# Kernel tuning notes

Hardware: AMD Instinct MI355X
Metric: run time of the kernel (lower is better)

The kernel has to match this reference:

```python
import jax, jax.numpy as jnp
import numpy as np

B, S, H = 2, 256, 512
EPS = 1e-12  # TPLinker conditional LayerNorm default epsilon
NEG = -1e30  # finite stand-in for -inf in running max


def _cond_layer_norm(x, cond, Wg, Wb, gamma, beta):
    # TPLinker conditional LayerNorm: gamma/beta are modulated by a linear map of cond.
    g = gamma + cond @ Wg          # (..., H)
    b = beta + cond @ Wb           # (..., H)
    xc = x - jnp.mean(x, axis=-1, keepdims=True)
    inv = jax.lax.rsqrt(jnp.mean(xc * xc, axis=-1, keepdims=True) + EPS)
    return xc * inv * g + b


def setup_inputs() -> dict:
    key = jax.random.key(0)
    ks = jax.random.split(key, 6)
    return {
        "seq_hiddens": jax.random.normal(ks[0], (B, S, H), jnp.float32),
        "mask": jnp.ones((B, S), jnp.float32),
        "lamtha": jax.random.uniform(ks[1], (H,), jnp.float32),
        "Wg1": jax.random.normal(ks[2], (H, H), jnp.float32) * 0.02,
        "Wb1": jax.random.normal(ks[3], (H, H), jnp.float32) * 0.02,
        "g1": jnp.ones((H,), jnp.float32),
        "b1": jnp.zeros((H,), jnp.float32),
        "Wg2": jax.random.normal(ks[4], (H, H), jnp.float32) * 0.02,
        "Wb2": jax.random.normal(ks[5], (H, H), jnp.float32) * 0.02,
        "g2": jnp.ones((H,), jnp.float32),
        "b2": jnp.zeros((H,), jnp.float32),
    }


def reference(seq_hiddens, mask, lamtha, Wg1, Wb1, g1, b1, Wg2, Wb2, g2, b2):
    # mask additive penalty, broadcast over hidden (matches (1-mask)*-1000 expand)
    seq = seq_hiddens + ((1.0 - mask) * -1000.0)[:, :, None]  # (B,S,H)

    ii, jj = jnp.triu_indices(S)  # row-major pairs (i, j>=i), same order as the torch loop

    # window means over seq[i..j] via cumulative sums (replaces O(S^3) recomputation)
    csum = jnp.cumsum(seq, axis=1)                              # (B,S,H)
    lens = (jj - ii + 1).astype(seq.dtype)[None, :, None]
    mean_pairs = (csum[:, jj] - csum[:, ii] + seq[:, ii]) / lens  # (B,P,H)

    # window maxes over seq[i..j]: scan over j keeping running max per start i
    idx = jnp.arange(S)

    def step(state, j):
        sj = jnp.take(seq, j, axis=1)  # (B,H)
        new = jnp.where((idx <= j)[None, :, None],
                        jnp.maximum(state, sj[:, None, :]),
                        jnp.asarray(NEG, seq.dtype))
        return new, new

    _, Mall = jax.lax.scan(step, jnp.full((B, S, H), NEG, seq.dtype), idx)  # (S_j,B,S_i,H)
    max_pairs = Mall[jj, :, ii].transpose(1, 0, 2)  # (B,P,H)

    # mix pooling
    inner = lamtha * mean_pairs + (1.0 - lamtha) * max_pairs  # (B,P,H)

    visible = seq[:, jj]  # (B,P,H) token j
    repeat = seq[:, ii]   # (B,P,H) token i

    shaking = _cond_layer_norm(visible, repeat, Wg1, Wb1, g1, b1)
    return _cond_layer_norm(shaking, inner, Wg2, Wb2, g2, b2)
```

## Files before the change

### kernel.cpp

```cpp
#include <hip/hip_runtime.h>
#include <hip/hip_bf16.h>

typedef __hip_bfloat16 bf16;
typedef short short8 __attribute__((ext_vector_type(8)));
typedef float floatx4 __attribute__((ext_vector_type(4)));

#define S 256
#define H 512
#define P 32896
#define NROWS 65792
#define NEGF -1e30f
#define EPSF 1e-12f

#define OFF_LN1    2129920u
#define OFF_G1     3178496u
#define OFF_B1     4227072u
#define OFF_WCAT   5275648u
#define OFF_II     6324224u
#define OFF_JJ     6390016u
#define OFF_MU2    6455808u
#define OFF_INV2   6718976u
#define OFF_INNER  6982144u

__device__ __forceinline__ void gld_lds16(const void* g, void* l) {
    __builtin_amdgcn_global_load_lds(
        (const __attribute__((address_space(1))) void*)g,
        (__attribute__((address_space(3))) void*)l, 16, 0, 0);
}

__global__ __launch_bounds__(512) void fusedA_kernel(
    const float* __restrict__ x, const float* __restrict__ mask,
    float* __restrict__ ln1,
    const float* __restrict__ Wg2, const float* __restrict__ Wb2,
    bf16* __restrict__ wcatT,
    unsigned short* __restrict__ ii, unsigned short* __restrict__ jj) {
    __shared__ float part[8][8][2];
    __shared__ float rstat[8][2];
    if (blockIdx.x < 64) {
        int b = blockIdx.x >> 5, sc = blockIdx.x & 31, h = threadIdx.x;
        int wave = h >> 6, lane = h & 63;
        int s0 = sc * 8;
        float v[8];
#pragma unroll
        for (int t = 0; t < 8; ++t) {
            int s = s0 + t;
            v[t] = x[(size_t)(b * S + s) * H + h] + (1.0f - mask[b * S + s]) * (-1000.0f);
        }
#pragma unroll
        for (int t = 0; t < 8; ++t) {
            float s = v[t], q = v[t] * v[t];
            for (int o = 1; o < 64; o <<= 1) { s += __shfl_xor(s, o); q += __shfl_xor(q, o); }
            if (lane == 0) { part[wave][t][0] = s; part[wave][t][1] = q; }
        }
        __syncthreads();
        if (h < 16) {
            int row = h >> 1, st = h & 1;
            float a = 0.0f;
#pragma unroll
            for (int w = 0; w < 8; ++w) a += part[w][row][st];
            rstat[row][st] = a;
        }
        __syncthreads();
#pragma unroll
        for (int t = 0; t < 8; ++t) {
            float m = rstat[t][0] * (1.0f / 512.0f);
            float var = rstat[t][1] * (1.0f / 512.0f) - m * m;
            var = var < 0.0f ? 0.0f : var;
            float inv = rsqrtf(var + EPSF);
            ln1[(size_t)(b * S + s0 + t) * H + h] = (v[t] - m) * inv;
        }
    } else {
        int n = blockIdx.x - 64;
        if (n < 1024) {
            int k = threadIdx.x;
            int tt = n >> 7, u = n & 127;
            int wnn = u >> 6, v = u & 63;
            int h = tt * 64 + wnn * 32 + (v & 31);
            float val = (v < 32) ? Wg2[(size_t)k * H + h] : Wb2[(size_t)k * H + h];
            wcatT[(size_t)n * H + k] = __float2bfloat16(val);
        } else {
            int p = (n - 1024) * 512 + threadIdx.x;
            if (p >= P) return;
            float disc = 513.0f * 513.0f - 8.0f * (float)p;
            int i = (int)((513.0f - sqrtf(disc)) * 0.5f);
            i = i < 0 ? 0 : (i > S - 1 ? S - 1 : i);
            while (i > 0 && (i * S - i * (i - 1) / 2) > p) --i;
            while (i < S - 1 && ((i + 1) * S - (i + 1) * i / 2) <= p) ++i;
            int off = i * S - i * (i - 1) / 2;
            ii[p] = (unsigned short)i;
            jj[p] = (unsigned short)(i + (p - off));
        }
    }
}

__global__ __launch_bounds__(256) void g1b1_kernel(
    const float* __restrict__ x, const float* __restrict__ mask,
    const float* __restrict__ Wg1, const float* __restrict__ Wb1,
    const float* __restrict__ g1, const float* __restrict__ b1,
    float* __restrict__ G1, float* __restrict__ B1) {
    __shared__ float rowbuf[4][H];
    int grp = blockIdx.x;
    int mat = blockIdx.y;
    int tid = threadIdx.x;
    int h0 = tid, h1 = tid + 256;
    int r0 = grp * 4;
#pragma unroll
    for (int r = 0; r < 4; ++r) {
        int row = r0 + r;
        float add = (1.0f - mask[row]) * (-1000.0f);
        rowbuf[r][h0] = x[(size_t)row * H + h0] + add;
        rowbuf[r][h1] = x[(size_t)row * H + h1] + add;
    }
    __syncthreads();
    const float* W = mat ? Wb1 : Wg1;
    float acc[4][2] = {{0, 0}, {0, 0}, {0, 0}, {0, 0}};
    for (int k8 = 0; k8 < 64; ++k8) {
        float4 ra[4][2];
#pragma unroll
        for (int r = 0; r < 4; ++r) {
            ra[r][0] = ((const float4*)rowbuf[r])[k8 * 2];
            ra[r][1] = ((const float4*)rowbuf[r])[k8 * 2 + 1];
        }
        float w0[8], w1[8];
#pragma unroll
        for (int kk = 0; kk < 8; ++kk) {
            w0[kk] = W[(size_t)(k8 * 8 + kk) * H + h0];
            w1[kk] = W[(size_t)(k8 * 8 + kk) * H + h1];
        }
#pragma unroll
        for (int r = 0; r < 4; ++r) {
            acc[r][0] += ra[r][0].x * w0[0] + ra[r][0].y * w0[1] +
                         ra[r][0].z * w0[2] + ra[r][0].w * w0[3] +
                         ra[r][1].x * w0[4] + ra[r][1].y * w0[5] +
                         ra[r][1].z * w0[6] + ra[r][1].w * w0[7];
            acc[r][1] += ra[r][0].x * w1[0] + ra[r][0].y * w1[1] +
                         ra[r][0].z * w1[2] + ra[r][0].w * w1[3] +
                         ra[r][1].x * w1[4] + ra[r][1].y * w1[5] +
                         ra[r][1].z * w1[6] + ra[r][1].w * w1[7];
        }
    }
    float bias0 = (mat ? b1 : g1)[h0];
    float bias1 = (mat ? b1 : g1)[h1];
    float* dst = mat ? B1 : G1;
#pragma unroll
    for (int r = 0; r < 4; ++r) {
        dst[(size_t)(r0 + r) * H + h0] = acc[r][0] + bias0;
        dst[(size_t)(r0 + r) * H + h1] = acc[r][1] + bias1;
    }
}

__global__ __launch_bounds__(256) void innerstats_kernel(
    const float* __restrict__ x, const float* __restrict__ mask,
    const float* __restrict__ lamtha,
    const float* __restrict__ ln1, const float* __restrict__ G1,
    const float* __restrict__ B1,
    bf16* __restrict__ inner, float* __restrict__ mu2, float* __restrict__ inv2) {
    __shared__ float sh_a[256];
    __shared__ float sh_b[256];
    int id = blockIdx.x;
    int kind = id & 1, sub = id >> 1;
    int t = sub & 255, b = sub >> 8;
    int i = b ? (255 - t) : t;
    int tid = threadIdx.x;
    int off = i * S - i * (i - 1) / 2;

    if (kind == 0) {
        int h2 = tid;
        sh_a[tid] = (1.0f - mask[b * S + tid]) * (-1000.0f);
        sh_b[tid] = 1.0f / (float)(tid + 1);
        __syncthreads();
        float2 lam = ((const float2*)lamtha)[h2];
        float2 oml = {1.0f - lam.x, 1.0f - lam.y};
        const float2* xb = (const float2*)(x + (size_t)b * S * H);
        float2 mrun = {NEGF, NEGF};
        float2 srun = {0.0f, 0.0f};
        size_t base = (size_t)b * P + (size_t)off;
        __hip_bfloat162* dst = (__hip_bfloat162*)inner;
        int j = i;
#define INNER_STEP(xx, jx)                                                 \
    {                                                                      \
        float ma = sh_a[jx];                                               \
        float vx = xx.x + ma, vy = xx.y + ma;                              \
        srun.x += vx;                                                      \
        srun.y += vy;                                                      \
        mrun.x = fmaxf(mrun.x, vx);                                        \
        mrun.y = fmaxf(mrun.y, vy);                                        \
        float rl = sh_b[(jx) - i];                                         \
        float fx = lam.x * (srun.x * rl) + oml.x * mrun.x;                 \
        float fy = lam.y * (srun.y * rl) + oml.y * mrun.y;                 \
        dst[(base + (size_t)((jx) - i)) * 256 + h2] =                      \
            __float22bfloat162_rn(make_float2(fx, fy));                    \
    }
        for (; j + 4 <= S; j += 4) {
            float2 x0 = xb[(j + 0) * 256 + h2];
            float2 x1 = xb[(j + 1) * 256 + h2];
            float2 x2 = xb[(j + 2) * 256 + h2];
            float2 x3 = xb[(j + 3) * 256 + h2];
            INNER_STEP(x0, j + 0)
            INNER_STEP(x1, j + 1)
            INNER_STEP(x2, j + 2)
            INNER_STEP(x3, j + 3)
        }
        for (; j < S; ++j) {
            float2 xv = xb[j * 256 + h2];
            INNER_STEP(xv, j)
        }
#undef INNER_STEP
    } else {
        int wave = tid >> 6, lane = tid & 63;
        const float4* gp = (const float4*)(G1 + (size_t)(b * S + i) * H);
        const float4* bp = (const float4*)(B1 + (size_t)(b * S + i) * H);
        float4 ga = gp[lane * 2], gb = gp[lane * 2 + 1];
        float4 ba = bp[lane * 2], bb = bp[lane * 2 + 1];
        for (int j = i + wave; j < S; j += 4) {
            const float4* lp = (const float4*)(ln1 + (size_t)(b * S + j) * H);
            float4 a0 = lp[lane * 2], a1 = lp[lane * 2 + 1];
            float v0 = a0.x * ga.x + ba.x, v1 = a0.y * ga.y + ba.y;
            float v2 = a0.z * ga.z + ba.z, v3 = a0.w * ga.w + ba.w;
            float v4 = a1.x * gb.x + bb.x, v5 = a1.y * gb.y + bb.y;
            float v6 = a1.z * gb.z + bb.z, v7 = a1.w * gb.w + bb.w;
            float sum = ((v0 + v1) + (v2 + v3)) + ((v4 + v5) + (v6 + v7));
            float ss = ((v0 * v0 + v1 * v1) + (v2 * v2 + v3 * v3)) +
                       ((v4 * v4 + v5 * v5) + (v6 * v6 + v7 * v7));
            for (int o = 1; o < 64; o <<= 1) { sum += __shfl_xor(sum, o); ss += __shfl_xor(ss, o); }
            if (lane == 0) {
                int r = b * P + off + (j - i);
                float m = sum * (1.0f / 512.0f);
                float var = ss * (1.0f / 512.0f) - m * m;
                var = var < 0.0f ? 0.0f : var;
                mu2[r] = m;
                inv2[r] = rsqrtf(var + EPSF);
            }
        }
    }
}

__global__ __launch_bounds__(256, 2) void gemm_kernel(
    const bf16* __restrict__ inner, const bf16* __restrict__ wcatT,
    const float* __restrict__ g2, const float* __restrict__ b2,
    const float* __restrict__ ln1, const float* __restrict__ G1, const float* __restrict__ B1,
    const unsigned short* __restrict__ ii, const unsigned short* __restrict__ jj,
    const float* __restrict__ mu2, const float* __restrict__ inv2,
    float* __restrict__ out) {
    extern __shared__ __align__(16) char smem[];

    const int tid = threadIdx.x;
    const int wave = tid >> 6, lane = tid & 63;
    const int q = lane >> 4, l15 = lane & 15;
    const int wm = wave & 1, wn = wave >> 1;

    const int id = blockIdx.x;
    int rb, t;
    if (id < 2048) { rb = (id >> 6) * 8 + (id & 7); t = (id >> 3) & 7; }
    else           { rb = 256; t = id - 2048; }
    const int R0 = rb * 256;

    int arow[4], acq[4];
#pragma unroll
    for (int s2 = 0; s2 < 4; ++s2) {
        int ci = s2 * 256 + tid;
        int pr = ci >> 3, pc = ci & 7, l = pc ^ (pr & 7);
        arow[s2] = (pr << 1) | (l >> 2);
        acq[s2] = l & 3;
    }
    const bf16* Asrc0 = inner + (size_t)(R0 + arow[0]) * H + acq[0] * 8;
    const bf16* Asrc1 = inner + (size_t)(R0 + arow[1]) * H + acq[1] * 8;
    const bf16* Asrc2 = inner + (size_t)(R0 + arow[2]) * H + acq[2] * 8;
    const bf16* Asrc3 = inner + (size_t)(R0 + arow[3]) * H + acq[3] * 8;
    const bf16* Bsrc0 = wcatT + (size_t)(t * 128 + arow[0]) * H + acq[0] * 8;
    const bf16* Bsrc1 = wcatT + (size_t)(t * 128 + arow[1]) * H + acq[1] * 8;

    char* const A0 = smem;
    char* const B0 = smem + 16384;
    char* const A1 = smem + 24576;
    char* const B1s = smem + 40960;

    const int prl = l15 >> 1;
    const int apc = ((((l15 & 1) << 2) | q) ^ prl) << 4;
    const int C = prl * 128 + apc;

    floatx4 acc[8][4];
#pragma unroll
    for (int a = 0; a < 8; ++a)
#pragma unroll
        for (int c = 0; c < 4; ++c) acc[a][c] = (floatx4){0.f, 0.f, 0.f, 0.f};

    auto STAGE = [&](int kt, char* Ad, char* Bd) {
        gld_lds16(Asrc0 + kt * 32, Ad + 0 * 4096 + wave * 1024);
        gld_lds16(Asrc1 + kt * 32, Ad + 1 * 4096 + wave * 1024);
        gld_lds16(Asrc2 + kt * 32, Ad + 2 * 4096 + wave * 1024);
        gld_lds16(Asrc3 + kt * 32, Ad + 3 * 4096 + wave * 1024);
        gld_lds16(Bsrc0 + kt * 32, Bd + 0 * 4096 + wave * 1024);
        gld_lds16(Bsrc1 + kt * 32, Bd + 1 * 4096 + wave * 1024);
    };

    STAGE(0, A0, B0);
    STAGE(1, A1, B1s);
    asm volatile("s_waitcnt vmcnt(6)" ::: "memory");
    asm volatile("s_barrier" ::: "memory");

#pragma unroll
    for (int kt = 0; kt < 16; ++kt) {
        char* const As = (kt & 1) ? A1 : A0;
        char* const Bs = (kt & 1) ? B1s : B0;

        short8 af[8], bfr[4];
#pragma unroll
        for (int fn = 0; fn < 4; ++fn)
            bfr[fn] = *(const short8*)(Bs + wn * 4096 + fn * 1024 + C);
#pragma unroll
        for (int fm = 0; fm < 8; ++fm)
            af[fm] = *(const short8*)(As + wm * 8192 + fm * 1024 + C);

        __builtin_amdgcn_s_setprio(1);
#pragma unroll
        for (int fm = 0; fm < 4; ++fm)
#pragma unroll
            for (int fn = 0; fn < 4; ++fn)
                acc[fm][fn] = __builtin_amdgcn_mfma_f32_16x16x32_bf16(af[fm], bfr[fn], acc[fm][fn], 0, 0, 0);
        __builtin_amdgcn_s_setprio(0);

        if (kt < 14) {
            asm volatile("s_waitcnt lgkmcnt(0)" ::: "memory");
            asm volatile("s_barrier" ::: "memory");
            STAGE(kt + 2, As, Bs);
        }

        __builtin_amdgcn_s_setprio(1);
#pragma unroll
        for (int fm = 4; fm < 8; ++fm)
#pragma unroll
            for (int fn = 0; fn < 4; ++fn)
                acc[fm][fn] = __builtin_amdgcn_mfma_f32_16x16x32_bf16(af[fm], bfr[fn], acc[fm][fn], 0, 0, 0);
        __builtin_amdgcn_s_setprio(0);

        if (kt < 14) {
            asm volatile("s_waitcnt vmcnt(6)" ::: "memory");
            asm volatile("s_barrier" ::: "memory");
        } else if (kt == 14) {
            asm volatile("s_waitcnt vmcnt(0)" ::: "memory");
            asm volatile("s_barrier" ::: "memory");
        }
    }

    float g2v[2], b2v[2];
#pragma unroll
    for (int fg = 0; fg < 2; ++fg) {
        int h = t * 64 + wn * 32 + fg * 16 + l15;
        g2v[fg] = g2[h];
        b2v[fg] = b2[h];
    }
#pragma unroll
    for (int fm = 0; fm < 8; ++fm) {
#pragma unroll
        for (int r = 0; r < 4; ++r) {
            int m = wm * 128 + fm * 16 + q * 4 + r;
            int rg = R0 + m;
            int b = (rg >= P) ? 1 : 0;
            int p = rg - b * P;
            int i = ii[p], j = jj[p];
            float mu = mu2[rg], iv = inv2[rg];
            const float* lp = ln1 + (size_t)(b * S + j) * H + t * 64 + wn * 32;
            const float* gp = G1 + (size_t)(b * S + i) * H + t * 64 + wn * 32;
            const float* bp = B1 + (size_t)(b * S + i) * H + t * 64 + wn * 32;
            float* op = out + (size_t)rg * H + t * 64 + wn * 32;
#pragma unroll
            for (int fg = 0; fg < 2; ++fg) {
                int c = fg * 16 + l15;
                float s = (lp[c] * gp[c] + bp[c] - mu) * iv;
                float G2v = acc[fm][fg][r] + g2v[fg];
                float B2v = acc[fm][fg + 2][r] + b2v[fg];
                op[c] = s * G2v + B2v;
            }
        }
    }
}

extern "C" void kernel_launch(void* const* d_in, const int* in_sizes, int n_in,
                              void* d_out, int out_size, void* d_ws, size_t ws_size,
                              hipStream_t stream) {
    const float* x = (const float*)d_in[0];
    const float* mask = (const float*)d_in[1];
    const float* lamtha = (const float*)d_in[2];
    const float* Wg1 = (const float*)d_in[3];
    const float* Wb1 = (const float*)d_in[4];
    const float* g1 = (const float*)d_in[5];
    const float* b1 = (const float*)d_in[6];
    const float* Wg2 = (const float*)d_in[7];
    const float* Wb2 = (const float*)d_in[8];
    const float* g2 = (const float*)d_in[9];
    const float* b2 = (const float*)d_in[10];
    float* out = (float*)d_out;

    char* ws = (char*)d_ws;
    float* ln1 = (float*)(ws + OFF_LN1);
    float* G1 = (float*)(ws + OFF_G1);
    float* B1 = (float*)(ws + OFF_B1);
    bf16* wcatT = (bf16*)(ws + OFF_WCAT);
    unsigned short* iiA = (unsigned short*)(ws + OFF_II);
    unsigned short* jjA = (unsigned short*)(ws + OFF_JJ);
    float* mu2 = (float*)(ws + OFF_MU2);
    float* inv2 = (float*)(ws + OFF_INV2);
    bf16* inner = (bf16*)(ws + OFF_INNER);

    static bool attr_set = false;
    if (!attr_set) {
        hipFuncSetAttribute((const void*)gemm_kernel,
                            hipFuncAttributeMaxDynamicSharedMemorySize, 49152);
        attr_set = true;
    }

    hipLaunchKernelGGL(fusedA_kernel, dim3(1153), dim3(512), 0, stream,
                       x, mask, ln1, Wg2, Wb2, wcatT, iiA, jjA);
    hipLaunchKernelGGL(g1b1_kernel, dim3(128, 2), dim3(256), 0, stream,
                       x, mask, Wg1, Wb1, g1, b1, G1, B1);
    hipLaunchKernelGGL(innerstats_kernel, dim3(1024), dim3(256), 0, stream,
                       x, mask, lamtha, ln1, G1, B1, inner, mu2, inv2);
    hipLaunchKernelGGL(gemm_kernel, dim3(2056), dim3(256), 49152, stream,
                       inner, wcatT, g2, b2, ln1, G1, B1, iiA, jjA, mu2, inv2, out);
}
```

Measured before the change: 306.9 us.

## Halve GEMM M-tile to 128 rows and reorder Wcat columns for occupancy

The main GEMM tile shrinks from 256x128 to 128x128. That halves LDS use and the accumulator registers, doubles the grid, and raises launch bounds to 3 blocks per CU. The transposed Wg2/Wb2 weight layout is reordered into contiguous 64-column gamma and beta halves, and the B-fragment LDS offsets are remapped to match. The aim is more resident waves to hide memory latency in an epilogue-heavy GEMM, at the cost of re-reading the B tile twice as often and lower per-block data reuse.

```diff
diff --git a/kernel.cpp b/kernel.cpp
--- a/kernel.cpp
+++ b/kernel.cpp
@@ -73,11 +73,10 @@
         int n = blockIdx.x - 64;
         if (n < 1024) {
             int k = threadIdx.x;
-            int tt = n >> 7, u = n & 127;
-            int wnn = u >> 6, v = u & 63;
-            int h = tt * 64 + wnn * 32 + (v & 31);
-            float val = (v < 32) ? Wg2[(size_t)k * H + h] : Wb2[(size_t)k * H + h];
-            wcatT[(size_t)n * H + k] = __float2bfloat16(val);
+            int tt = n >> 7, c = n & 127;
+            int h = tt * 64 + (c & 63);
+            float v = (c < 64) ? Wg2[(size_t)k * H + h] : Wb2[(size_t)k * H + h];
+            wcatT[(size_t)n * H + k] = __float2bfloat16(v);
         } else {
             int p = (n - 1024) * 512 + threadIdx.x;
             if (p >= P) return;
@@ -235,7 +234,7 @@
     }
 }
 
-__global__ __launch_bounds__(256, 2) void gemm_kernel(
+__global__ __launch_bounds__(256, 3) void gemm_kernel(
     const bf16* __restrict__ inner, const bf16* __restrict__ wcatT,
     const float* __restrict__ g2, const float* __restrict__ b2,
     const float* __restrict__ ln1, const float* __restrict__ G1, const float* __restrict__ B1,
@@ -251,52 +250,48 @@
 
     const int id = blockIdx.x;
     int rb, t;
-    if (id < 2048) { rb = (id >> 6) * 8 + (id & 7); t = (id >> 3) & 7; }
-    else           { rb = 256; t = id - 2048; }
-    const int R0 = rb * 256;
-
-    int arow[4], acq[4];
-#pragma unroll
-    for (int s2 = 0; s2 < 4; ++s2) {
+    if (id < 4096) { rb = (id >> 6) * 8 + (id & 7); t = (id >> 3) & 7; }
+    else           { int w = id - 4096; rb = 512 + (w & 1); t = w >> 1; }
+    const int R0 = rb * 128;
+
+    int arow[2], acq[2];
+#pragma unroll
+    for (int s2 = 0; s2 < 2; ++s2) {
         int ci = s2 * 256 + tid;
         int pr = ci >> 3, pc = ci & 7, l = pc ^ (pr & 7);
         arow[s2] = (pr << 1) | (l >> 2);
         acq[s2] = l & 3;
     }
-    const bf16* Asrc0 = inner + (size_t)(R0 + arow[0]) * H + acq[0] * 8;
-    const bf16* Asrc1 = inner + (size_t)(R0 + arow[1]) * H + acq[1] * 8;
-    const bf16* Asrc2 = inner + (size_t)(R0 + arow[2]) * H + acq[2] * 8;
-    const bf16* Asrc3 = inner + (size_t)(R0 + arow[3]) * H + acq[3] * 8;
-    const bf16* Bsrc0 = wcatT + (size_t)(t * 128 + arow[0]) * H + acq[0] * 8;
-    const bf16* Bsrc1 = wcatT + (size_t)(t * 128 + arow[1]) * H + acq[1] * 8;
+    const bf16* const Asrc0 = inner + (size_t)(R0 + arow[0]) * H + acq[0] * 8;
+    const bf16* const Asrc1 = inner + (size_t)(R0 + arow[1]) * H + acq[1] * 8;
+    const bf16* const Bsrc0 = wcatT + (size_t)(t * 128 + arow[0]) * H + acq[0] * 8;
+    const bf16* const Bsrc1 = wcatT + (size_t)(t * 128 + arow[1]) * H + acq[1] * 8;
 
     char* const A0 = smem;
-    char* const B0 = smem + 16384;
-    char* const A1 = smem + 24576;
-    char* const B1s = smem + 40960;
+    char* const B0 = smem + 8192;
+    char* const A1 = smem + 16384;
+    char* const B1s = smem + 24576;
 
     const int prl = l15 >> 1;
     const int apc = ((((l15 & 1) << 2) | q) ^ prl) << 4;
     const int C = prl * 128 + apc;
 
-    floatx4 acc[8][4];
-#pragma unroll
-    for (int a = 0; a < 8; ++a)
+    floatx4 acc[4][4];
+#pragma unroll
+    for (int a = 0; a < 4; ++a)
 #pragma unroll
         for (int c = 0; c < 4; ++c) acc[a][c] = (floatx4){0.f, 0.f, 0.f, 0.f};
 
     auto STAGE = [&](int kt, char* Ad, char* Bd) {
-        gld_lds16(Asrc0 + kt * 32, Ad + 0 * 4096 + wave * 1024);
-        gld_lds16(Asrc1 + kt * 32, Ad + 1 * 4096 + wave * 1024);
-        gld_lds16(Asrc2 + kt * 32, Ad + 2 * 4096 + wave * 1024);
-        gld_lds16(Asrc3 + kt * 32, Ad + 3 * 4096 + wave * 1024);
-        gld_lds16(Bsrc0 + kt * 32, Bd + 0 * 4096 + wave * 1024);
-        gld_lds16(Bsrc1 + kt * 32, Bd + 1 * 4096 + wave * 1024);
+        gld_lds16(Asrc0 + kt * 32, Ad + wave * 1024);
+        gld_lds16(Asrc1 + kt * 32, Ad + 4096 + wave * 1024);
+        gld_lds16(Bsrc0 + kt * 32, Bd + wave * 1024);
+        gld_lds16(Bsrc1 + kt * 32, Bd + 4096 + wave * 1024);
     };
 
     STAGE(0, A0, B0);
     STAGE(1, A1, B1s);
-    asm volatile("s_waitcnt vmcnt(6)" ::: "memory");
+    asm volatile("s_waitcnt vmcnt(4)" ::: "memory");
     asm volatile("s_barrier" ::: "memory");
 
 #pragma unroll
@@ -304,17 +299,20 @@
         char* const As = (kt & 1) ? A1 : A0;
         char* const Bs = (kt & 1) ? B1s : B0;
 
-        short8 af[8], bfr[4];
-#pragma unroll
-        for (int fn = 0; fn < 4; ++fn)
-            bfr[fn] = *(const short8*)(Bs + wn * 4096 + fn * 1024 + C);
-#pragma unroll
-        for (int fm = 0; fm < 8; ++fm)
-            af[fm] = *(const short8*)(As + wm * 8192 + fm * 1024 + C);
+        short8 af[4], bfr[4];
+#pragma unroll
+        for (int fn = 0; fn < 4; ++fn) {
+            int boff = (fn < 2) ? (wn * 2048 + fn * 1024)
+                                : (4096 + wn * 2048 + (fn - 2) * 1024);
+            bfr[fn] = *(const short8*)(Bs + boff + C);
+        }
+#pragma unroll
+        for (int fm = 0; fm < 4; ++fm)
+            af[fm] = *(const short8*)(As + wm * 4096 + fm * 1024 + C);
 
         __builtin_amdgcn_s_setprio(1);
 #pragma unroll
-        for (int fm = 0; fm < 4; ++fm)
+        for (int fm = 0; fm < 2; ++fm)
 #pragma unroll
             for (int fn = 0; fn < 4; ++fn)
                 acc[fm][fn] = __builtin_amdgcn_mfma_f32_16x16x32_bf16(af[fm], bfr[fn], acc[fm][fn], 0, 0, 0);
@@ -328,14 +326,14 @@
 
         __builtin_amdgcn_s_setprio(1);
 #pragma unroll
-        for (int fm = 4; fm < 8; ++fm)
+        for (int fm = 2; fm < 4; ++fm)
 #pragma unroll
             for (int fn = 0; fn < 4; ++fn)
                 acc[fm][fn] = __builtin_amdgcn_mfma_f32_16x16x32_bf16(af[fm], bfr[fn], acc[fm][fn], 0, 0, 0);
         __builtin_amdgcn_s_setprio(0);
 
         if (kt < 14) {
-            asm volatile("s_waitcnt vmcnt(6)" ::: "memory");
+            asm volatile("s_waitcnt vmcnt(4)" ::: "memory");
             asm volatile("s_barrier" ::: "memory");
         } else if (kt == 14) {
             asm volatile("s_waitcnt vmcnt(0)" ::: "memory");
@@ -351,10 +349,10 @@
         b2v[fg] = b2[h];
     }
 #pragma unroll
-    for (int fm = 0; fm < 8; ++fm) {
+    for (int fm = 0; fm < 4; ++fm) {
 #pragma unroll
         for (int r = 0; r < 4; ++r) {
-            int m = wm * 128 + fm * 16 + q * 4 + r;
+            int m = wm * 64 + fm * 16 + q * 4 + r;
             int rg = R0 + m;
             int b = (rg >= P) ? 1 : 0;
             int p = rg - b * P;
@@ -406,7 +404,7 @@
     static bool attr_set = false;
     if (!attr_set) {
         hipFuncSetAttribute((const void*)gemm_kernel,
-                            hipFuncAttributeMaxDynamicSharedMemorySize, 49152);
+                            hipFuncAttributeMaxDynamicSharedMemorySize, 32768);
         attr_set = true;
     }
 
@@ -416,6 +414,6 @@
                        x, mask, Wg1, Wb1, g1, b1, G1, B1);
     hipLaunchKernelGGL(innerstats_kernel, dim3(1024), dim3(256), 0, stream,
                        x, mask, lamtha, ln1, G1, B1, inner, mu2, inv2);
-    hipLaunchKernelGGL(gemm_kernel, dim3(2056), dim3(256), 49152, stream,
+    hipLaunchKernelGGL(gemm_kernel, dim3(4112), dim3(256), 32768, stream,
                        inner, wcatT, g2, b2, ln1, G1, B1, iiA, jjA, mu2, inv2, out);
 }
```

Result: no change. 305.9 us (-0.3%).
